# Optimization experiments

Measured on AMD Instinct MI355X. Metric: run time of the kernel, lower is better.

The kernel has to match this reference:

```python
import jax, jax.numpy as jnp
import numpy as np

NX, NY = 432, 496  # BEV grid from cfg ranges / voxel size
EPS = 1e-5


def _bn(x, g, b, m, v):
    # eval-mode batchnorm, channel on last axis of the param broadcast
    return (x - m) / jnp.sqrt(v + EPS) * g + b


def setup_inputs() -> dict:
    key = jax.random.key(0)
    ks = jax.random.split(key, 24)
    B, P, N, C = 4, 12000, 32, 9
    pillars = jax.random.normal(ks[0], (B, P, N, C), jnp.float32)

    # unique (x, y) pillar coords per batch via permutation of grid cells
    def coords_for(k):
        cells = jax.random.permutation(k, NY * NX)[:P]
        y = cells // NX
        x = cells % NX
        return jnp.stack([x, y], axis=-1)

    coords = jax.vmap(coords_for)(jax.random.split(ks[1], B)).astype(jnp.int32)
    coords = coords.at[:, P - P // 10:, :].set(0)
    num_points = jax.random.randint(ks[2], (B, P), 0, N, jnp.int32)

    def bn_params(k, c):
        k1, k2, k3, k4 = jax.random.split(k, 4)
        return (jax.random.uniform(k1, (c,), jnp.float32) + 0.5,
                jax.random.normal(k2, (c,), jnp.float32) * 0.1,
                jax.random.normal(k3, (c,), jnp.float32) * 0.1,
                jax.random.uniform(k4, (c,), jnp.float32) + 0.5)

    pfn_w = jax.random.normal(ks[3], (64, 9), jnp.float32) * 0.1
    pfn_g, pfn_b, pfn_m, pfn_v = bn_params(ks[4], 64)
    w1 = jax.random.normal(ks[5], (64, 64, 3, 3), jnp.float32) * 0.05
    g1, b1, m1, v1 = bn_params(ks[6], 64)
    w2 = jax.random.normal(ks[7], (128, 64, 3, 3), jnp.float32) * 0.05
    g2, b2, m2, v2 = bn_params(ks[8], 128)
    num_classes, num_anchors = 3, 2
    cls_w = jax.random.normal(ks[9], (num_classes * num_anchors, 128), jnp.float32) * 0.05
    cls_b = jax.random.normal(ks[10], (num_classes * num_anchors,), jnp.float32) * 0.01
    reg_w = jax.random.normal(ks[11], (7 * num_anchors, 128), jnp.float32) * 0.05
    reg_b = jax.random.normal(ks[12], (7 * num_anchors,), jnp.float32) * 0.01
    dir_w = jax.random.normal(ks[13], (2 * num_anchors, 128), jnp.float32) * 0.05
    dir_b = jax.random.normal(ks[14], (2 * num_anchors,), jnp.float32) * 0.01

    return dict(pillars=pillars, coords=coords, num_points=num_points,
                pfn_w=pfn_w, pfn_g=pfn_g, pfn_b=pfn_b, pfn_m=pfn_m, pfn_v=pfn_v,
                w1=w1, g1=g1, b1=b1, m1=m1, v1=v1,
                w2=w2, g2=g2, b2=b2, m2=m2, v2=v2,
                cls_w=cls_w, cls_b=cls_b, reg_w=reg_w, reg_b=reg_b,
                dir_w=dir_w, dir_b=dir_b)


def _conv(x, w, stride):
    # ZeroPad2d(1) + Conv2d(pad=0) == conv with explicit (1,1) padding
    return jax.lax.conv_general_dilated(
        x, w, (stride, stride), [(1, 1), (1, 1)],
        dimension_numbers=('NCHW', 'OIHW', 'NCHW'))


def _bn_nchw(x, g, b, m, v):
    r = lambda p: p[None, :, None, None]
    return (x - r(m)) / jnp.sqrt(r(v) + EPS) * r(g) + r(b)


def reference(pillars, coords, num_points,
              pfn_w, pfn_g, pfn_b, pfn_m, pfn_v,
              w1, g1, b1, m1, v1, w2, g2, b2, m2, v2,
              cls_w, cls_b, reg_w, reg_b, dir_w, dir_b):
    B, P, N, C = pillars.shape
    # --- PillarFeatureNet: 1x1 conv over C, BN, ReLU, max over points ---
    feat = jnp.einsum('bpnc,oc->bpno', pillars, pfn_w)          # [B,P,N,64]
    feat = jax.nn.relu(_bn(feat, pfn_g, pfn_b, pfn_m, pfn_v))
    feat = feat.max(axis=2)                                      # [B,P,64]

    # --- vectorized scatter into dense BEV canvas (replaces python loop) ---
    valid = coords.sum(axis=-1) != 0                             # [B,P]
    xi = coords[..., 0]
    yi = jnp.where(valid, coords[..., 1], NY)                    # OOB -> dropped
    bi = jnp.broadcast_to(jnp.arange(B)[:, None], (B, P))
    canvas = jnp.zeros((B, NY, NX, feat.shape[-1]), feat.dtype)
    canvas = canvas.at[bi, yi, xi].set(feat, mode='drop')
    canvas = canvas.transpose(0, 3, 1, 2)                        # [B,64,NY,NX]

    # --- Backbone ---
    x = jax.nn.relu(_bn_nchw(_conv(canvas, w1, 2), g1, b1, m1, v1))  # [B,64,248,216]
    x = jax.nn.relu(_bn_nchw(_conv(x, w2, 1), g2, b2, m2, v2))       # [B,128,248,216]

    # --- Detection heads (1x1 convs) ---
    def head(w, b):
        return jnp.einsum('bchw,oc->bohw', x, w) + b[None, :, None, None]

    cls_preds = head(cls_w, cls_b)   # [B,6,248,216]
    reg_preds = head(reg_w, reg_b)   # [B,14,248,216]
    dir_preds = head(dir_w, dir_b)   # [B,4,248,216]
    return cls_preds, reg_preds, dir_preds
```

## Files before the change

### kernel.cpp

```cpp
#include <hip/hip_runtime.h>

#define BATCH 4
#define NPIL 12000
#define NPTS 32
#define NCH 9
#define NXg 432
#define NYg 496
#define OHh 248
#define OWw 216
#define HWp (OHh*OWw)
#define CAN_STRIDE ((size_t)NYg*NXg*64)
#define X1_STRIDE  ((size_t)OHh*OWw*64)
#define MASKW 8192

typedef __bf16 bf16x8 __attribute__((ext_vector_type(8)));
typedef float  f32x4  __attribute__((ext_vector_type(4)));

__device__ __forceinline__ bf16x8 as_bf16x8(uint4 u) {
    union { uint4 u; bf16x8 b; } c; c.u = u; return c.b;
}

__device__ __forceinline__ float b2f(unsigned int u) {
    union { unsigned int i; float f; } x; x.i = (u & 0xffffu) << 16; return x.f;
}
__device__ __forceinline__ unsigned short f2b(float f) {
    union { float f; unsigned int i; } x; x.f = f;
    unsigned int r = x.i + 0x7fffu + ((x.i >> 16) & 1u);
    return (unsigned short)(r >> 16);
}
__device__ __forceinline__ float ldin(const void* p, int i, int isbf) {
    return isbf ? b2f(((const unsigned short*)p)[i]) : ((const float*)p)[i];
}

__device__ __forceinline__ void async_load16(const void* gsrc, void* ldst) {
    __builtin_amdgcn_global_load_lds(
        (const __attribute__((address_space(1))) unsigned char*)gsrc,
        (__attribute__((address_space(3))) unsigned char*)ldst, 16, 0, 0);
}

__global__ void sentinel_kernel(float* out, float val) {
    if (threadIdx.x == 0) out[0] = val;
}

__device__ __forceinline__ int plaus16(unsigned short h) {
    if ((h & 0x7fffu) == 0) return 1;
    unsigned e = (h >> 7) & 0xffu;
    return (e >= 106 && e <= 132) ? 1 : 0;
}

__global__ __launch_bounds__(256) void prep_weights(
    const void* q0,  const void* q1,  const void* q2,  const void* q3,
    const void* q4,  const void* q5,  const void* q6,  const void* q7,
    const void* q8,  const void* q9,  const void* q10, const void* q11,
    const void* q12, const void* q13, const void* q14, const void* q15,
    const void* q16, const void* q17, const void* q18, const void* q19,
    const void* q20, const void* q21,
    unsigned short* __restrict__ wt1, unsigned short* __restrict__ wt2,
    unsigned short* __restrict__ whh, unsigned short* __restrict__ whl,
    unsigned int* __restrict__ mask, int mask_words,
    unsigned int* __restrict__ zbuf,
    int* __restrict__ flags_out)
{
    __shared__ int votes[22];
    __shared__ int sflags[24];
    const void* ptrs[22] = {q0,q1,q2,q3,q4,q5,q6,q7,q8,q9,q10,q11,
                            q12,q13,q14,q15,q16,q17,q18,q19,q20,q21};
    const int Ks[22]   = {64,64,32,32,32,32,64,32,32,32,32,64,64,64,64,64,64,3,64,7,64,2};
    const int didx[22] = {0,3,4,5,6,7,8,9,10,11,12,13,14,15,16,17,18,19,20,21,22,23};
    const int tid = threadIdx.x;
    if (tid < 22) votes[tid] = 0;
    if (tid < 24) sflags[tid] = 0;
    __syncthreads();
    #pragma unroll 1
    for (int wb = 0; wb < 4; ++wb) {
        const int vt = wb*256 + tid;
        int off = 0;
        #pragma unroll
        for (int t = 0; t < 22; ++t) {
            if (vt >= off && vt < off + Ks[t]) {
                unsigned w = ((const unsigned*)ptrs[t])[vt - off];
                if (plaus16((unsigned short)w) && plaus16((unsigned short)(w >> 16)))
                    atomicAdd(&votes[t], 1);
            }
            off += Ks[t];
        }
    }
    __syncthreads();
    if (tid < 22) {
        int isbf;
        if (tid == 17 || tid == 19 || tid == 21) {
            int pv = votes[17] + votes[19] + votes[21];
            isbf = (pv * 4 >= 3 * 12);
        } else {
            isbf = (votes[tid] * 4 >= 3 * Ks[tid]);
        }
        sflags[didx[tid]] = isbf;
    }
    __syncthreads();
    if (blockIdx.x == 0 && tid < 24) flags_out[tid] = sflags[tid];

    const int f1 = sflags[8], f2 = sflags[13];
    int i = blockIdx.x * 256 + tid;
    if (i < mask_words) mask[i] = 0u;
    if (i < 16) zbuf[i] = 0u;
    if (i < 64*64*9) {
        int kx = i % 3; int t = i / 3; int ky = t % 3; t /= 3; int ic = t % 64; int oc = t / 64;
        wt1[((size_t)(ky*3 + kx)*64 + oc)*64 + ic] = f2b(ldin(q6, i, f1));
    }
    if (i < 128*64*9) {
        int kx = i % 3; int t = i / 3; int ky = t % 3; t /= 3; int ic = t % 64; int oc = t / 64;
        wt2[((size_t)(ky*3 + kx)*128 + oc)*64 + ic] = f2b(ldin(q11, i, f2));
    }
    if (i < 32*128) {
        int ic = i & 127, o = i >> 7;
        float wv = 0.f;
        if (o < 6)       wv = ldin(q16, o*128 + ic, sflags[18]);
        else if (o < 20) wv = ldin(q18, (o-6)*128 + ic, sflags[20]);
        else if (o < 24) wv = ldin(q20, (o-20)*128 + ic, sflags[22]);
        unsigned short hi = f2b(wv);
        whh[i] = hi;
        whl[i] = f2b(wv - b2f(hi));
    }
}

__global__ __launch_bounds__(256) void pfn_scatter(
    const void* __restrict__ pillars, const int* __restrict__ coords,
    const void* __restrict__ pfn_w,
    const void* __restrict__ g, const void* __restrict__ bb,
    const void* __restrict__ m, const void* __restrict__ v,
    const int* __restrict__ flags, int b0,
    unsigned int* __restrict__ mask,
    unsigned short* __restrict__ canvas)
{
    __shared__ float lds[4][NPTS*NCH];
    const int wslot = threadIdx.x >> 6;
    const int lane  = threadIdx.x & 63;
    const int p = blockIdx.x * 4 + wslot;
    const int b = b0 + blockIdx.y;
    canvas += (size_t)blockIdx.y * CAN_STRIDE;
    mask   += (size_t)blockIdx.y * MASKW;
    const size_t pg = (size_t)b * NPIL + p;

    if (flags[0]) {
        const unsigned short* src = (const unsigned short*)pillars + pg * (NPTS*NCH);
        for (int idx = lane; idx < NPTS*NCH; idx += 64) lds[wslot][idx] = b2f(src[idx]);
    } else {
        const float4* src = (const float4*)((const float*)pillars + pg * (NPTS*NCH));
        for (int idx = lane; idx < (NPTS*NCH)/4; idx += 64)
            *(float4*)&lds[wslot][idx*4] = src[idx];
    }
    float w[NCH];
    const int fW = flags[3];
    #pragma unroll
    for (int c = 0; c < NCH; ++c) w[c] = ldin(pfn_w, lane*NCH + c, fW);
    float s = ldin(g, lane, flags[4]) / sqrtf(ldin(v, lane, flags[7]) + 1e-5f);
    float t = ldin(bb, lane, flags[5]) - ldin(m, lane, flags[6]) * s;
    __syncthreads();

    float mx = 0.0f;
    #pragma unroll 4
    for (int n = 0; n < NPTS; ++n) {
        const float* r = &lds[wslot][n*NCH];
        float acc = r[0] * w[0];
        #pragma unroll
        for (int c = 1; c < NCH; ++c) acc = fmaf(r[c], w[c], acc);
        mx = fmaxf(mx, fmaxf(fmaf(acc, s, t), 0.0f));
    }
    const int cx = coords[pg*2], cy = coords[pg*2 + 1];
    if (cx + cy != 0 && cx >= 0 && cx < NXg && cy >= 0 && cy < NYg) {
        const int cell = cy*NXg + cx;
        canvas[(size_t)cell*64 + lane] = f2b(mx);
        if (lane == 0) atomicOr(&mask[cell >> 5], 1u << (cell & 31));
    }
}

#define LDB1(buf, tap, ks) { \
    _Pragma("unroll") \
    for (int j_ = 0; j_ < 4; ++j_) \
        buf[j_] = *(const uint4*)&wt[((size_t)((tap)*64 + j_*16 + lr))*64 + (ks)*32 + lg*8]; \
}

__global__ __launch_bounds__(256, 2) void conv1_mfma(
    const unsigned short* __restrict__ canvas,
    const unsigned int* __restrict__ mask,
    const unsigned short* __restrict__ wt,
    const uint4* __restrict__ zbuf,
    const void* __restrict__ g, const void* __restrict__ bb,
    const void* __restrict__ m, const void* __restrict__ v,
    const int* __restrict__ flags,
    unsigned short* __restrict__ x1)
{
    __shared__ __align__(16) uint4 lin[16*33*8];
    const int tid = threadIdx.x;
    const int w = tid >> 6, l = tid & 63;
    const int lr = l & 15, lg = l >> 4;
    const int px0 = blockIdx.x * 16, oy0 = blockIdx.y * 16;
    canvas += (size_t)blockIdx.z * CAN_STRIDE;
    mask   += (size_t)blockIdx.z * MASKW;
    x1     += (size_t)blockIdx.z * X1_STRIDE;

    f32x4 acc[4][4];
    #pragma unroll
    for (int t = 0; t < 4; ++t)
        #pragma unroll
        for (int n = 0; n < 4; ++n) acc[t][n] = (f32x4){0.f,0.f,0.f,0.f};

    uint4 wbA[4], wbB[4];
    LDB1(wbA, 0, 0);

    #pragma unroll 1
    for (int ky = 0; ky < 3; ++ky) {
        __syncthreads();
        for (int q = tid; q < 16*33*8; q += 256) {
            int s = q & 7, t2 = q >> 3, c = t2 % 33, r = t2 / 33;
            int iy = 2*oy0 + ky - 1 + 2*r, gx = 2*px0 - 1 + c;
            const void* src = zbuf;
            if ((unsigned)iy < (unsigned)NYg && (unsigned)gx < (unsigned)NXg) {
                const int cell = iy*NXg + gx;
                if ((mask[cell >> 5] >> (cell & 31)) & 1u)
                    src = &canvas[(size_t)cell*64 + (s ^ ((c >> 1) & 7))*8];
            }
            async_load16(src, &lin[q]);
        }
        __syncthreads();
        #pragma unroll 1
        for (int kx = 0; kx < 3; ++kx) {
            const int tap = ky*3 + kx;
            const int c = 2*lr + kx;
            const int key = (c >> 1) & 7;
            LDB1(wbB, tap, 1);
            __builtin_amdgcn_s_setprio(1);
            #pragma unroll
            for (int t = 0; t < 4; ++t) {
                const int base = ((4*w + t)*33 + c)*8;
                bf16x8 a0 = as_bf16x8(lin[base + (lg ^ key)]);
                #pragma unroll
                for (int n = 0; n < 4; ++n)
                    acc[t][n] = __builtin_amdgcn_mfma_f32_16x16x32_bf16(a0, as_bf16x8(wbA[n]), acc[t][n], 0, 0, 0);
            }
            __builtin_amdgcn_s_setprio(0);
            if (tap < 8) LDB1(wbA, tap + 1, 0);
            __builtin_amdgcn_s_setprio(1);
            #pragma unroll
            for (int t = 0; t < 4; ++t) {
                const int base = ((4*w + t)*33 + c)*8;
                bf16x8 a1 = as_bf16x8(lin[base + ((4 + lg) ^ key)]);
                #pragma unroll
                for (int n = 0; n < 4; ++n)
                    acc[t][n] = __builtin_amdgcn_mfma_f32_16x16x32_bf16(a1, as_bf16x8(wbB[n]), acc[t][n], 0, 0, 0);
            }
            __builtin_amdgcn_s_setprio(0);
        }
    }
    float s[4], tt[4];
    #pragma unroll
    for (int n = 0; n < 4; ++n) {
        const int oc = n*16 + lr;
        s[n]  = ldin(g, oc, flags[9]) / sqrtf(ldin(v, oc, flags[12]) + 1e-5f);
        tt[n] = ldin(bb, oc, flags[10]) - ldin(m, oc, flags[11]) * s[n];
    }
    #pragma unroll
    for (int t = 0; t < 4; ++t) {
        const int oy = oy0 + 4*w + t;
        if (oy >= OHh) continue;
        #pragma unroll
        for (int r = 0; r < 4; ++r) {
            const int px = px0 + lg*4 + r;
            if (px >= OWw) continue;
            unsigned short* orow = &x1[((size_t)oy*OWw + px)*64 + lr];
            #pragma unroll
            for (int n = 0; n < 4; ++n)
                orow[n*16] = f2b(fmaxf(fmaf(acc[t][n][r], s[n], tt[n]), 0.f));
        }
    }
}

__global__ __launch_bounds__(256, 2) void conv2_mfma(
    const unsigned short* __restrict__ x1,
    const unsigned short* __restrict__ wt,
    const unsigned short* __restrict__ whh,
    const unsigned short* __restrict__ whl,
    const uint4* __restrict__ zbuf,
    const void* __restrict__ g, const void* __restrict__ bb,
    const void* __restrict__ m, const void* __restrict__ v,
    const void* __restrict__ cls_b, const void* __restrict__ reg_b, const void* __restrict__ dir_b,
    const int* __restrict__ flags, int b0,
    float* __restrict__ out)
{
    __shared__ __align__(16) char smem[74240];
    uint4* lin = (uint4*)smem;
    uint4 (*lw)[128*8] = (uint4 (*)[128*8])(smem + 41472);
    unsigned short* P = (unsigned short*)smem;

    const int tid = threadIdx.x;
    const int w = tid >> 6, l = tid & 63;
    const int lr = l & 15, lg = l >> 4;
    const int px0 = blockIdx.x * 16, oy0 = blockIdx.y * 16;
    const int b = b0 + blockIdx.z;
    x1 += (size_t)blockIdx.z * X1_STRIDE;

    for (int q = tid; q < 18*18*8; q += 256) {
        int s = q & 7, t2 = q >> 3, c = t2 % 18, r = t2 / 18;
        int iy = oy0 - 1 + r, gx = px0 - 1 + c;
        const void* src = zbuf;
        if ((unsigned)iy < (unsigned)OHh && (unsigned)gx < (unsigned)OWw)
            src = &x1[((size_t)(iy*OWw + gx))*64 + (s ^ (c & 7))*8];
        async_load16(src, &lin[q]);
    }
    #pragma unroll
    for (int i = 0; i < 4; ++i) {
        const int q = tid + i*256, oc = q >> 3, s = q & 7;
        async_load16(&wt[((size_t)oc)*64 + (s ^ (oc & 7))*8], &lw[0][q]);
    }
    __syncthreads();

    f32x4 acc[4][8];
    #pragma unroll
    for (int t = 0; t < 4; ++t)
        #pragma unroll
        for (int n = 0; n < 8; ++n) acc[t][n] = (f32x4){0.f,0.f,0.f,0.f};

    #pragma unroll 1
    for (int tap = 0; tap < 9; ++tap) {
        const int ky = tap / 3, kx = tap - 3*ky;
        const int cur = tap & 1;
        if (tap < 8) {
            #pragma unroll
            for (int i = 0; i < 4; ++i) {
                const int q = tid + i*256, oc = q >> 3, s = q & 7;
                async_load16(&wt[((size_t)((tap+1)*128 + oc))*64 + (s ^ (oc & 7))*8],
                             &lw[cur ^ 1][q]);
            }
        }
        const int c = lr + kx;
        const int key = c & 7;
        bf16x8 af[4][2];
        #pragma unroll
        for (int t = 0; t < 4; ++t) {
            const int base = ((4*w + t + ky)*18 + c)*8;
            af[t][0] = as_bf16x8(lin[base + (lg ^ key)]);
            af[t][1] = as_bf16x8(lin[base + ((4 + lg) ^ key)]);
        }
        __builtin_amdgcn_s_setprio(1);
        #pragma unroll
        for (int n = 0; n < 8; ++n) {
            const int oc = n*16 + lr;
            const bf16x8 b0 = as_bf16x8(lw[cur][oc*8 + (lg ^ (oc & 7))]);
            const bf16x8 b1 = as_bf16x8(lw[cur][oc*8 + ((4 + lg) ^ (oc & 7))]);
            #pragma unroll
            for (int t = 0; t < 4; ++t) {
                acc[t][n] = __builtin_amdgcn_mfma_f32_16x16x32_bf16(af[t][0], b0, acc[t][n], 0, 0, 0);
                acc[t][n] = __builtin_amdgcn_mfma_f32_16x16x32_bf16(af[t][1], b1, acc[t][n], 0, 0, 0);
            }
        }
        __builtin_amdgcn_s_setprio(0);
        __syncthreads();
    }

    float s[8], tt[8];
    #pragma unroll
    for (int n = 0; n < 8; ++n) {
        const int oc = n*16 + lr;
        s[n]  = ldin(g, oc, flags[14]) / sqrtf(ldin(v, oc, flags[17]) + 1e-5f);
        tt[n] = ldin(bb, oc, flags[15]) - ldin(m, oc, flags[16]) * s[n];
    }

    float bias0, bias1;
    {
        int o = lr;
        bias0 = (o < 6) ? ldin(cls_b, o, flags[19]) : ldin(reg_b, o - 6, flags[21]);
        o = 16 + lr;
        bias1 = (o < 20) ? ldin(reg_b, o - 6, flags[21])
              : (o < 24) ? ldin(dir_b, o - 20, flags[23]) : 0.f;
    }
    uint4 wh[2][4], wl[2][4];
    #pragma unroll
    for (int n = 0; n < 2; ++n)
        #pragma unroll
        for (int ks = 0; ks < 4; ++ks) {
            const int ei = (n*16 + lr)*128 + ks*32 + lg*8;
            wh[n][ks] = *(const uint4*)&whh[ei];
            wl[n][ks] = *(const uint4*)&whl[ei];
        }

    __syncthreads();
    #pragma unroll
    for (int t = 0; t < 4; ++t) {
        const int pb = ((4*w + t)*16 + lg*4) * 128;
        #pragma unroll
        for (int n = 0; n < 8; ++n) {
            const int kk = 2*n + (lr >> 3), wi = lr & 7;
            #pragma unroll
            for (int r = 0; r < 4; ++r) {
                float val = fmaxf(fmaf(acc[t][n][r], s[n], tt[n]), 0.f);
                unsigned short h = f2b(val);
                P[pb + r*128 + ((kk ^ (lg*4 + r)) << 3) + wi] = h;
                acc[t][n][r] = val - b2f(h);
            }
        }
    }
    __syncthreads();

    f32x4 hacc[4][2];
    #pragma unroll
    for (int t = 0; t < 4; ++t) {
        hacc[t][0] = (f32x4){bias0, bias0, bias0, bias0};
        hacc[t][1] = (f32x4){bias1, bias1, bias1, bias1};
    }
    #pragma unroll
    for (int t = 0; t < 4; ++t) {
        const int mt = 4*w + t;
        bf16x8 pa[4];
        #pragma unroll
        for (int ks = 0; ks < 4; ++ks)
            pa[ks] = as_bf16x8(((const uint4*)P)[(mt*16 + lr)*16 + ((ks*4 + lg) ^ lr)]);
        #pragma unroll
        for (int n = 0; n < 2; ++n)
            #pragma unroll
            for (int ks = 0; ks < 4; ++ks) {
                hacc[t][n] = __builtin_amdgcn_mfma_f32_16x16x32_bf16(pa[ks], as_bf16x8(wh[n][ks]), hacc[t][n], 0, 0, 0);
                hacc[t][n] = __builtin_amdgcn_mfma_f32_16x16x32_bf16(pa[ks], as_bf16x8(wl[n][ks]), hacc[t][n], 0, 0, 0);
            }
    }
    __syncthreads();
    #pragma unroll
    for (int t = 0; t < 4; ++t) {
        const int pb = ((4*w + t)*16 + lg*4) * 128;
        #pragma unroll
        for (int n = 0; n < 8; ++n) {
            const int kk = 2*n + (lr >> 3), wi = lr & 7;
            #pragma unroll
            for (int r = 0; r < 4; ++r)
                P[pb + r*128 + ((kk ^ (lg*4 + r)) << 3) + wi] = f2b(acc[t][n][r]);
        }
    }
    __syncthreads();
    #pragma unroll
    for (int t = 0; t < 4; ++t) {
        const int mt = 4*w + t;
        bf16x8 pa[4];
        #pragma unroll
        for (int ks = 0; ks < 4; ++ks)
            pa[ks] = as_bf16x8(((const uint4*)P)[(mt*16 + lr)*16 + ((ks*4 + lg) ^ lr)]);
        #pragma unroll
        for (int n = 0; n < 2; ++n)
            #pragma unroll
            for (int ks = 0; ks < 4; ++ks)
                hacc[t][n] = __builtin_amdgcn_mfma_f32_16x16x32_bf16(pa[ks], as_bf16x8(wh[n][ks]), hacc[t][n], 0, 0, 0);
    }

    const size_t regbase = (size_t)BATCH*6*HWp;
    const size_t dirbase = regbase + (size_t)BATCH*14*HWp;
    const int pxw = px0 + lg*4;
    #pragma unroll
    for (int n = 0; n < 2; ++n) {
        const int o = n*16 + lr;
        float* plane;
        bool valid = (pxw < OWw);
        if (o < 6)       plane = out + ((size_t)b*6 + o)*HWp;
        else if (o < 20) plane = out + regbase + ((size_t)b*14 + (o - 6))*HWp;
        else if (o < 24) plane = out + dirbase + ((size_t)b*4 + (o - 20))*HWp;
        else valid = false;
        if (!valid) continue;
        #pragma unroll
        for (int t = 0; t < 4; ++t) {
            const int oy = oy0 + 4*w + t;
            if (oy < OHh)
                *(float4*)&plane[(size_t)oy*OWw + pxw] = *(float4*)&hacc[t][n];
        }
    }
}

extern "C" void kernel_launch(void* const* d_in, const int* in_sizes, int n_in,
                              void* d_out, int out_size, void* d_ws, size_t ws_size,
                              hipStream_t stream) {
    static const int EXPECT[24] = {13824000,96000,48000,576,64,64,64,64,36864,
                                   64,64,64,64,73728,128,128,128,128,768,6,1792,14,512,4};
    const void* din[24];
    {
        bool used[24] = {false};
        int perm[24];
        bool ok = (n_in >= 24);
        if (ok) {
            for (int j = 0; j < 24 && ok; ++j) {
                perm[j] = -1;
                for (int i = 0; i < 24; ++i)
                    if (!used[i] && in_sizes[i] == EXPECT[j]) { perm[j] = i; used[i] = true; break; }
                if (perm[j] < 0) ok = false;
            }
        }
        for (int j = 0; j < 24; ++j) din[j] = d_in[ok ? perm[j] : j];
        if (!ok) {
            sentinel_kernel<<<1, 64, 0, stream>>>((float*)d_out, 13000.0f + n_in);
            return;
        }
    }
    const int* coords = (const int*)din[1];
    float* out = (float*)d_out;

    const size_t X1B   = (size_t)HWp*64*2;
    const size_t CANB  = (size_t)NYg*NXg*64*2;
    const size_t MASKB = (size_t)MASKW*4;
    const size_t ZOFF  = 256 + 73728 + 147456 + 8192 + 8192;
    const size_t BASE  = ZOFF + 64;
    const size_t NEED1 = BASE + MASKB + X1B + CANB;
    const size_t NEED4 = BASE + 4*(MASKB + X1B + CANB);
    if (ws_size < NEED1) {
        sentinel_kernel<<<1, 64, 0, stream>>>(out, 10000.0f + (float)(ws_size >> 20));
        return;
    }
    const int nb = (ws_size >= NEED4) ? 4 : 1;
    char* ws = (char*)d_ws;
    int* flags = (int*)ws;
    unsigned short* wt1 = (unsigned short*)(ws + 256);
    unsigned short* wt2 = (unsigned short*)(ws + 256 + 73728);
    unsigned short* whh = (unsigned short*)(ws + 256 + 73728 + 147456);
    unsigned short* whl = (unsigned short*)(ws + 256 + 73728 + 147456 + 8192);
    unsigned int*   zbuf = (unsigned int*)(ws + ZOFF);
    unsigned int*   maskbuf = (unsigned int*)(ws + BASE);
    unsigned short* x1  = (unsigned short*)(ws + BASE + (size_t)nb*MASKB);
    unsigned short* canvas = (unsigned short*)(ws + BASE + (size_t)nb*(MASKB + X1B));

    prep_weights<<<288, 256, 0, stream>>>(
        din[0], din[3], din[4], din[5], din[6], din[7],
        din[8], din[9], din[10], din[11], din[12],
        din[13], din[14], din[15], din[16], din[17],
        din[18], din[19], din[20], din[21], din[22], din[23],
        wt1, wt2, whh, whl, maskbuf, nb*MASKW, zbuf, flags);

    if (nb == 4) {
        pfn_scatter<<<dim3(NPIL/4, 4), 256, 0, stream>>>(
            din[0], coords, din[3], din[4], din[5], din[6], din[7], flags, 0, maskbuf, canvas);
        conv1_mfma<<<dim3(14, 16, 4), 256, 0, stream>>>(
            canvas, maskbuf, wt1, (const uint4*)zbuf,
            din[9], din[10], din[11], din[12], flags, x1);
        conv2_mfma<<<dim3(14, 16, 4), 256, 0, stream>>>(
            x1, wt2, whh, whl, (const uint4*)zbuf, din[14], din[15], din[16], din[17],
            din[19], din[21], din[23], flags, 0, out);
    } else {
        for (int b = 0; b < BATCH; ++b) {
            if (b) hipMemsetAsync(maskbuf, 0, MASKB, stream);
            pfn_scatter<<<dim3(NPIL/4, 1), 256, 0, stream>>>(
                din[0], coords, din[3], din[4], din[5], din[6], din[7], flags, b, maskbuf, canvas);
            conv1_mfma<<<dim3(14, 16, 1), 256, 0, stream>>>(
                canvas, maskbuf, wt1, (const uint4*)zbuf,
                din[9], din[10], din[11], din[12], flags, x1);
            conv2_mfma<<<dim3(14, 16, 1), 256, 0, stream>>>(
                x1, wt2, whh, whl, (const uint4*)zbuf, din[14], din[15], din[16], din[17],
                din[19], din[21], din[23], flags, b, out);
        }
    }
}
```

Measured before the change: 334.4 us.

## Share even input rows between ky=0 and ky=2 taps in conv1 staging

With stride 2, the input rows for ky=0 and ky=2 overlap: ky=2 row r equals ky=0 row r+1. The conv1 kernel now stages 17 even-offset rows once and runs taps from both ky=0 and ky=2 against them with a row offset, then stages the odd rows for ky=1. This cuts the LDS fill passes from three to two and removes about a third of the redundant global/mask loads and barriers. In exchange, LDS use rises (17 rows instead of 16), which may affect occupancy at two blocks per CU, and the tap order and weight prefetch sequence become more intricate.

After: 329.8 us. No clear change (-1.4%).

```diff
diff --git a/kernel.cpp b/kernel.cpp
--- a/kernel.cpp
+++ b/kernel.cpp
@@ -190,7 +190,7 @@
     const int* __restrict__ flags,
     unsigned short* __restrict__ x1)
 {
-    __shared__ __align__(16) uint4 lin[16*33*8];
+    __shared__ __align__(16) uint4 lin[17*33*8];
     const int tid = threadIdx.x;
     const int w = tid >> 6, l = tid & 63;
     const int lr = l & 15, lg = l >> 4;
@@ -208,42 +208,43 @@
     uint4 wbA[4], wbB[4];
     LDB1(wbA, 0, 0);
 
-    #pragma unroll 1
-    for (int ky = 0; ky < 3; ++ky) {
-        __syncthreads();
-        for (int q = tid; q < 16*33*8; q += 256) {
-            int s = q & 7, t2 = q >> 3, c = t2 % 33, r = t2 / 33;
-            int iy = 2*oy0 + ky - 1 + 2*r, gx = 2*px0 - 1 + c;
-            const void* src = zbuf;
-            if ((unsigned)iy < (unsigned)NYg && (unsigned)gx < (unsigned)NXg) {
-                const int cell = iy*NXg + gx;
-                if ((mask[cell >> 5] >> (cell & 31)) & 1u)
-                    src = &canvas[(size_t)cell*64 + (s ^ ((c >> 1) & 7))*8];
-            }
-            async_load16(src, &lin[q]);
-        }
-        __syncthreads();
-        #pragma unroll 1
-        for (int kx = 0; kx < 3; ++kx) {
-            const int tap = ky*3 + kx;
+    for (int q = tid; q < 17*33*8; q += 256) {
+        int s = q & 7, t2 = q >> 3, c = t2 % 33, j = t2 / 33;
+        int iy = 2*oy0 - 1 + 2*j, gx = 2*px0 - 1 + c;
+        const void* src = zbuf;
+        if ((unsigned)iy < (unsigned)NYg && (unsigned)gx < (unsigned)NXg) {
+            const int cell = iy*NXg + gx;
+            if ((mask[cell >> 5] >> (cell & 31)) & 1u)
+                src = &canvas[(size_t)cell*64 + (s ^ ((c >> 1) & 7))*8];
+        }
+        async_load16(src, &lin[q]);
+    }
+    __syncthreads();
+    {
+        const int SEQA[6] = {0, 6, 1, 7, 2, 8};
+        #pragma unroll
+        for (int i = 0; i < 6; ++i) {
+            const int tap = SEQA[i];
+            const int kx = tap % 3;
+            const int joff = (tap >= 6) ? 1 : 0;
             const int c = 2*lr + kx;
             const int key = (c >> 1) & 7;
             LDB1(wbB, tap, 1);
             __builtin_amdgcn_s_setprio(1);
             #pragma unroll
             for (int t = 0; t < 4; ++t) {
-                const int base = ((4*w + t)*33 + c)*8;
+                const int base = ((4*w + t + joff)*33 + c)*8;
                 bf16x8 a0 = as_bf16x8(lin[base + (lg ^ key)]);
                 #pragma unroll
                 for (int n = 0; n < 4; ++n)
                     acc[t][n] = __builtin_amdgcn_mfma_f32_16x16x32_bf16(a0, as_bf16x8(wbA[n]), acc[t][n], 0, 0, 0);
             }
             __builtin_amdgcn_s_setprio(0);
-            if (tap < 8) LDB1(wbA, tap + 1, 0);
+            LDB1(wbA, (i < 5) ? SEQA[i + 1] : 3, 0);
             __builtin_amdgcn_s_setprio(1);
             #pragma unroll
             for (int t = 0; t < 4; ++t) {
-                const int base = ((4*w + t)*33 + c)*8;
+                const int base = ((4*w + t + joff)*33 + c)*8;
                 bf16x8 a1 = as_bf16x8(lin[base + ((4 + lg) ^ key)]);
                 #pragma unroll
                 for (int n = 0; n < 4; ++n)
@@ -252,6 +253,49 @@
             __builtin_amdgcn_s_setprio(0);
         }
     }
+
+    __syncthreads();
+    for (int q = tid; q < 16*33*8; q += 256) {
+        int s = q & 7, t2 = q >> 3, c = t2 % 33, j = t2 / 33;
+        int iy = 2*oy0 + 2*j, gx = 2*px0 - 1 + c;
+        const void* src = zbuf;
+        if ((unsigned)iy < (unsigned)NYg && (unsigned)gx < (unsigned)NXg) {
+            const int cell = iy*NXg + gx;
+            if ((mask[cell >> 5] >> (cell & 31)) & 1u)
+                src = &canvas[(size_t)cell*64 + (s ^ ((c >> 1) & 7))*8];
+        }
+        async_load16(src, &lin[q]);
+    }
+    __syncthreads();
+    #pragma unroll
+    for (int tap = 3; tap < 6; ++tap) {
+        const int kx = tap - 3;
+        const int c = 2*lr + kx;
+        const int key = (c >> 1) & 7;
+        LDB1(wbB, tap, 1);
+        __builtin_amdgcn_s_setprio(1);
+        #pragma unroll
+        for (int t = 0; t < 4; ++t) {
+            const int base = ((4*w + t)*33 + c)*8;
+            bf16x8 a0 = as_bf16x8(lin[base + (lg ^ key)]);
+            #pragma unroll
+            for (int n = 0; n < 4; ++n)
+                acc[t][n] = __builtin_amdgcn_mfma_f32_16x16x32_bf16(a0, as_bf16x8(wbA[n]), acc[t][n], 0, 0, 0);
+        }
+        __builtin_amdgcn_s_setprio(0);
+        if (tap < 5) LDB1(wbA, tap + 1, 0);
+        __builtin_amdgcn_s_setprio(1);
+        #pragma unroll
+        for (int t = 0; t < 4; ++t) {
+            const int base = ((4*w + t)*33 + c)*8;
+            bf16x8 a1 = as_bf16x8(lin[base + ((4 + lg) ^ key)]);
+            #pragma unroll
+            for (int n = 0; n < 4; ++n)
+                acc[t][n] = __builtin_amdgcn_mfma_f32_16x16x32_bf16(a1, as_bf16x8(wbB[n]), acc[t][n], 0, 0, 0);
+        }
+        __builtin_amdgcn_s_setprio(0);
+    }
+
     float s[4], tt[4];
     #pragma unroll
     for (int n = 0; n < 4; ++n) {
```
